# Kernel tuning notes

Hardware: AMD Instinct MI355X
Metric: run time of the kernel (lower is better)

## Reference

```python
import jax, jax.numpy as jnp
import numpy as np

M, B, T, C, H, HS = 2, 8, 1024, 512, 8, 64
EPS = 1e-5

NAMES = ['x','sa_kw1','sa_kb1','sa_kw2','sa_qw1','sa_qb1','sa_qw2','sa_vw1','sa_vb1','sa_vw2',
         'sa_pw1','sa_pb1','sa_pw2','sa_pb2','ff_w1','ff_b1','ff_w2','ff_b2',
         'ln1_g','ln1_b','ln2_g','ln2_b','lnc_g','lnc_b',
         'ca_qw','ca_kvw','ca_pw1','ca_pb1','ca_pw2','ca_pb2']


def setup_inputs() -> dict:
    key = jax.random.key(0)
    it = iter(jax.random.split(key, 40))
    def w(shape, s=0.02):
        return jax.random.normal(next(it), shape, jnp.float32) * s
    d = {}
    d['x'] = jax.random.normal(next(it), (M, B, T, C), jnp.float32)
    # self-attention heads: Linear(C,HS//2)+bias -> tanh -> Linear(HS//2,HS) no bias, stacked over (M,H)
    for nm in ('k', 'q', 'v'):
        d['sa_%sw1' % nm] = w((M, H, C, HS // 2))
        d['sa_%sb1' % nm] = jnp.zeros((M, H, HS // 2), jnp.float32)
        d['sa_%sw2' % nm] = w((M, H, HS // 2, HS))
    # MHA output proj: Linear(H*HS,C//2)->tanh->Linear(C//2,C)
    d['sa_pw1'] = w((M, H * HS, C // 2)); d['sa_pb1'] = jnp.zeros((M, C // 2), jnp.float32)
    d['sa_pw2'] = w((M, C // 2, C));      d['sa_pb2'] = jnp.zeros((M, C), jnp.float32)
    # feed-forward
    d['ff_w1'] = w((M, C, 4 * C)); d['ff_b1'] = jnp.zeros((M, 4 * C), jnp.float32)
    d['ff_w2'] = w((M, 4 * C, C)); d['ff_b2'] = jnp.zeros((M, C), jnp.float32)
    # layernorms
    for nm in ('ln1', 'ln2', 'lnc'):
        d[nm + '_g'] = jnp.ones((M, C), jnp.float32)
        d[nm + '_b'] = jnp.zeros((M, C), jnp.float32)
    # cross-attention: per head q proj (no bias), per-kv-modality kv proj (no bias, 2*HS)
    d['ca_qw'] = w((M, H, C, HS))
    d['ca_kvw'] = w((M, H, M - 1, C, 2 * HS))
    d['ca_pw1'] = w((M, H * HS, C // 2)); d['ca_pb1'] = jnp.zeros((M, C // 2), jnp.float32)
    d['ca_pw2'] = w((M, C // 2, C));      d['ca_pb2'] = jnp.zeros((M, C), jnp.float32)
    return d


def _ln(x, g, b):
    mu = x.mean(-1, keepdims=True)
    var = ((x - mu) ** 2).mean(-1, keepdims=True)
    return (x - mu) * jax.lax.rsqrt(var + EPS) * g + b


def _attend(q, k, v, mask):
    # q,k,v: (B,H,T,HS); causal masked softmax attention
    aff = jnp.einsum('bhtd,bhsd->bhts', q, k) * (HS ** -0.5)
    aff = jnp.where(mask, aff, -jnp.inf)
    return jnp.einsum('bhts,bhsd->bhtd', jax.nn.softmax(aff, axis=-1), v)


def _merge(o):
    # (B,H,T,HS) -> (B,T,H*HS), matching torch.cat over heads
    return o.transpose(0, 2, 1, 3).reshape(o.shape[0], o.shape[2], -1)


def _forward(p):
    mask = jnp.tril(jnp.ones((T, T), bool))
    x = p['x']
    attended = []
    for i in range(M):  # fixed small modality loop
        xi = x[i]
        h = _ln(xi, p['ln1_g'][i], p['ln1_b'][i])
        def hm(w1, b1, w2):
            # batched over heads: Linear->tanh->Linear
            z = jnp.tanh(jnp.einsum('btc,hce->bhte', h, w1) + b1[:, None, :])
            return jnp.einsum('bhte,hed->bhtd', z, w2)
        o = _attend(hm(p['sa_qw1'][i], p['sa_qb1'][i], p['sa_qw2'][i]),
                    hm(p['sa_kw1'][i], p['sa_kb1'][i], p['sa_kw2'][i]),
                    hm(p['sa_vw1'][i], p['sa_vb1'][i], p['sa_vw2'][i]), mask)
        o = jnp.tanh(_merge(o) @ p['sa_pw1'][i] + p['sa_pb1'][i]) @ p['sa_pw2'][i] + p['sa_pb2'][i]
        xi = xi + o
        h2 = _ln(xi, p['ln2_g'][i], p['ln2_b'][i])
        xi = xi + (jax.nn.relu(h2 @ p['ff_w1'][i] + p['ff_b1'][i]) @ p['ff_w2'][i] + p['ff_b2'][i])
        attended.append(xi)
    outs = []
    for i in range(M):
        xi = attended[i]
        hq = _ln(xi, p['lnc_g'][i], p['lnc_b'][i])
        q = jnp.einsum('btc,hcd->bhtd', hq, p['ca_qw'][i])
        acc = 0.0
        for jidx, j in enumerate([j for j in range(M) if j != i]):
            kv = jnp.einsum('btc,hcd->bhtd', attended[j], p['ca_kvw'][i][:, jidx])
            k, v = jnp.split(kv, 2, axis=-1)
            acc = acc + _attend(q, k, v, mask)
        o = jnp.tanh(_merge(acc) @ p['ca_pw1'][i] + p['ca_pb1'][i]) @ p['ca_pw2'][i] + p['ca_pb2'][i]
        outs.append(xi + o)
    return jnp.stack(outs)


def reference(x, sa_kw1, sa_kb1, sa_kw2, sa_qw1, sa_qb1, sa_qw2, sa_vw1, sa_vb1, sa_vw2,
              sa_pw1, sa_pb1, sa_pw2, sa_pb2, ff_w1, ff_b1, ff_w2, ff_b2,
              ln1_g, ln1_b, ln2_g, ln2_b, lnc_g, lnc_b,
              ca_qw, ca_kvw, ca_pw1, ca_pb1, ca_pw2, ca_pb2):
    args = (x, sa_kw1, sa_kb1, sa_kw2, sa_qw1, sa_qb1, sa_qw2, sa_vw1, sa_vb1, sa_vw2,
            sa_pw1, sa_pb1, sa_pw2, sa_pb2, ff_w1, ff_b1, ff_w2, ff_b2,
            ln1_g, ln1_b, ln2_g, ln2_b, lnc_g, lnc_b,
            ca_qw, ca_kvw, ca_pw1, ca_pb1, ca_pw2, ca_pb2)
    return _forward(dict(zip(NAMES, args)))
```

## Files before the change

### kernel.cpp

```cpp
#include <hip/hip_runtime.h>
#include <hip/hip_bf16.h>

#define DEVI __device__ __forceinline__

typedef __attribute__((ext_vector_type(8))) short short8v;
typedef __attribute__((ext_vector_type(4))) float float4v;
typedef __attribute__((ext_vector_type(16))) float f32x16;

#if defined(__has_builtin)
#if __has_builtin(__builtin_amdgcn_exp2f)
#define EXP2F(x) __builtin_amdgcn_exp2f(x)
#endif
#endif
#ifndef EXP2F
#define EXP2F(x) exp2f(x)
#endif

constexpr int Mm = 2, Bb = 8, Tt = 1024, Cc = 512, Hh = 8, HSs = 64;
constexpr int ROWS = Bb * Tt;
constexpr size_t BTC = (size_t)Bb * Tt * Cc;
constexpr size_t SLAB = (size_t)ROWS * 512;
constexpr size_t KOFF = (size_t)2 * ROWS * 768;
constexpr size_t VOFF = KOFF + 2 * SLAB;
constexpr float SCQ = 0.18033688011112042f;

DEVI short f2bf(float f) {
    __hip_bfloat16 h = __float2bfloat16(f);
    short s; __builtin_memcpy(&s, &h, 2); return s;
}

DEVI float4v mfma16(short8v a, short8v b, float4v c) {
    return __builtin_amdgcn_mfma_f32_16x16x32_bf16(a, b, c, 0, 0, 0);
}
DEVI f32x16 mfma32(short8v a, short8v b, f32x16 c) {
    return __builtin_amdgcn_mfma_f32_32x32x16_bf16(a, b, c, 0, 0, 0);
}

DEVI void gload_lds16(const short* g, short* l) {
    __builtin_amdgcn_global_load_lds(
        (const __attribute__((address_space(1))) void*)g,
        (__attribute__((address_space(3))) void*)l, 16, 0, 0);
}

__global__ __launch_bounds__(256) void transpose_cvt(const float* __restrict__ src,
                                                     short* __restrict__ dst,
                                                     int K, int N, size_t moff, size_t hoff) {
    __shared__ float t[32][33];
    int k0 = blockIdx.x * 32, n0 = blockIdx.y * 32;
    int z = blockIdx.z;
    size_t so = (size_t)z * K * N;
    short* d = dst + (size_t)(z >> 3) * moff + (size_t)(z & 7) * hoff;
    int tx = threadIdx.x, ty = threadIdx.y;
#pragma unroll
    for (int i = 0; i < 32; i += 8)
        t[ty + i][tx] = src[so + (size_t)(k0 + ty + i) * N + n0 + tx];
    __syncthreads();
#pragma unroll
    for (int i = 0; i < 32; i += 8)
        d[(size_t)(n0 + ty + i) * K + k0 + tx] = f2bf(t[tx][ty + i]);
}

__global__ __launch_bounds__(256) void bias_cat3(const float* __restrict__ q,
                                                 const float* __restrict__ k,
                                                 const float* __restrict__ v,
                                                 float* __restrict__ o) {
    int m = blockIdx.x, t = threadIdx.x;
    o[m * 768 + t]       = q[m * 256 + t];
    o[m * 768 + 256 + t] = k[m * 256 + t];
    o[m * 768 + 512 + t] = v[m * 256 + t];
}

__global__ __launch_bounds__(256) void vtrans(const short* __restrict__ V,
                                              short* __restrict__ VT,
                                              int vrs, int hs, long long vzs) {
    __shared__ short t[32][33];
    int t0 = blockIdx.x * 32, d0 = blockIdx.y * 32;
    int z = blockIdx.z, mod = z >> 6, bh = z & 63, b = bh >> 3, h = bh & 7;
    const short* src = V + (long long)mod * vzs + (size_t)b * Tt * vrs + h * hs;
    short* dst = VT + (size_t)z * 65536;
    int tx = threadIdx.x, ty = threadIdx.y;
#pragma unroll
    for (int i = 0; i < 32; i += 8)
        t[ty + i][tx] = src[(size_t)(t0 + ty + i) * vrs + d0 + tx];
    __syncthreads();
#pragma unroll
    for (int i = 0; i < 32; i += 8)
        dst[(size_t)(d0 + ty + i) * Tt + t0 + tx] = t[tx][ty + i];
}

__global__ __launch_bounds__(256) void ln_kernel(const float* __restrict__ x,
                                                 const float* __restrict__ g,
                                                 const float* __restrict__ b,
                                                 short* __restrict__ out, size_t xzs) {
    __shared__ float ssum[4], ssq[4];
    int z = blockIdx.y;
    x += z * xzs; g += z * Cc; b += z * Cc; out += z * SLAB;
    int row = blockIdx.x, tid = threadIdx.x;
    const float* xr = x + (size_t)row * Cc;
    float v0 = xr[tid], v1 = xr[tid + 256];
    float s = v0 + v1, q = v0 * v0 + v1 * v1;
#pragma unroll
    for (int o = 1; o < 64; o <<= 1) { s += __shfl_xor(s, o, 64); q += __shfl_xor(q, o, 64); }
    int w = tid >> 6;
    if ((tid & 63) == 0) { ssum[w] = s; ssq[w] = q; }
    __syncthreads();
    s = ssum[0] + ssum[1] + ssum[2] + ssum[3];
    q = ssq[0] + ssq[1] + ssq[2] + ssq[3];
    float mu = s * (1.f / Cc);
    float var = q * (1.f / Cc) - mu * mu;
    float rs = rsqrtf(var + 1e-5f);
    short* orow = out + (size_t)row * Cc;
    orow[tid]       = f2bf((v0 - mu) * rs * g[tid]       + b[tid]);
    orow[tid + 256] = f2bf((v1 - mu) * rs * g[tid + 256] + b[tid + 256]);
}

template<int ACT, bool BIAS, bool RES, bool WF, bool WB>
__global__ __launch_bounds__(256, 2) void gemm3(
    const short* __restrict__ A, int lda, long long a_zs,
    const short* __restrict__ Wt, int ldw, long long w_zs,
    const float* __restrict__ bias, long long bias_zs,
    const float* __restrict__ res, long long res_zs,
    float* __restrict__ outF, long long outF_zs,
    short* __restrict__ outB, long long outB_zs,
    int ldc, int K, float oscale) {
    constexpr int BM = 128, BN = 128, BK = 64;
    __shared__ short As[2][BM][BK];
    __shared__ short Bs[2][BN][BK];
    long long z = blockIdx.z;
    A += z * a_zs; Wt += z * w_zs;
    if (BIAS) bias += z * bias_zs;
    if (RES)  res  += z * res_zs;
    if (WF)   outF += z * outF_zs;
    if (WB)   outB += z * outB_zs;
    int m0 = blockIdx.x * BM, n0 = blockIdx.y * BN;
    int tid = threadIdx.x, wv = tid >> 6, l = tid & 63;
    int lq = l & 31, hi = l >> 5;
    int wm = wv & 1, wn = wv >> 1;
    f32x16 acc[2][2] = {};
    int lrow = l >> 3;
    int gcol = (l & 7) ^ lrow;

    auto STAGE = [&](int bi, int k0) {
#pragma unroll
        for (int c = 0; c < 4; c++) {
            int ch = wv + c * 4;
            gload_lds16(&A[(size_t)(m0 + ch * 8 + lrow) * lda + k0 + gcol * 8],
                        &As[bi][ch * 8][0]);
        }
#pragma unroll
        for (int c = 0; c < 4; c++) {
            int ch = wv + c * 4;
            gload_lds16(&Wt[(size_t)(n0 + ch * 8 + lrow) * ldw + k0 + gcol * 8],
                        &Bs[bi][ch * 8][0]);
        }
    };

    STAGE(0, 0);
    __syncthreads();
    int NT = K / BK;
    for (int t = 0; t < NT; t++) {
        int cur = t & 1;
        if (t + 1 < NT) STAGE(cur ^ 1, (t + 1) * BK);
        const short (*Ac)[BK] = As[cur];
        const short (*Bc)[BK] = Bs[cur];
#pragma unroll
        for (int ks = 0; ks < 4; ks++) {
            int g = (ks * 2 + hi) ^ (lq & 7);
            short8v af[2], bf[2];
#pragma unroll
            for (int i = 0; i < 2; i++)
                af[i] = *(const short8v*)&Ac[wm * 64 + i * 32 + lq][g * 8];
#pragma unroll
            for (int j = 0; j < 2; j++)
                bf[j] = *(const short8v*)&Bc[wn * 64 + j * 32 + lq][g * 8];
#pragma unroll
            for (int i = 0; i < 2; i++)
#pragma unroll
                for (int j = 0; j < 2; j++)
                    acc[i][j] = mfma32(af[i], bf[j], acc[i][j]);
        }
        __syncthreads();
    }
#pragma unroll
    for (int i = 0; i < 2; i++) {
#pragma unroll
        for (int j = 0; j < 2; j++) {
            int col = n0 + wn * 64 + j * 32 + lq;
            float bv = BIAS ? bias[col] : 0.f;
#pragma unroll
            for (int r = 0; r < 16; r++) {
                int row = m0 + wm * 64 + i * 32 + 4 * hi + (r & 3) + 8 * (r >> 2);
                float v = acc[i][j][r] * oscale + bv;
                if (ACT == 1) v = tanhf(v);
                if (ACT == 2) v = fmaxf(v, 0.f);
                size_t idx = (size_t)row * ldc + col;
                if (RES) v += res[idx];
                if (WF) outF[idx] = v;
                if (WB) outB[idx] = f2bf(v);
            }
        }
    }
}

template<int BM, int BN, int ACT, bool BIAS, bool RES, bool WF, bool WB>
__global__ __launch_bounds__(256, 2) void gemm2(
    const short* __restrict__ A, int lda, long long a_zs,
    const short* __restrict__ Wt, int ldw, long long w_zs,
    const float* __restrict__ bias, long long bias_zs,
    const float* __restrict__ res, long long res_zs,
    float* __restrict__ outF, long long outF_zs,
    short* __restrict__ outB, long long outB_zs,
    int ldc, int K, float oscale) {
    constexpr int BK = 64;
    __shared__ short As[BM][BK];
    __shared__ short Bs[BN][BK];
    long long z = blockIdx.z;
    A += z * a_zs; Wt += z * w_zs;
    if (BIAS) bias += z * bias_zs;
    if (RES)  res  += z * res_zs;
    if (WF)   outF += z * outF_zs;
    if (WB)   outB += z * outB_zs;
    int m0 = blockIdx.x * BM, n0 = blockIdx.y * BN;
    int tid = threadIdx.x, wv = tid >> 6, l = tid & 63, lr = l & 15, lg = l >> 4;
    constexpr int WM = BM / 2, WN = BN / 2;
    int wm = wv & 1, wn = wv >> 1;
    constexpr int AI = WM / 16, BJ = WN / 16;
    float4v acc[AI][BJ] = {};
    int lrow = l >> 3;
    int gcol = (l & 7) ^ lrow;
    constexpr int CHA = BM / 8, CHB = BN / 8;
    for (int k0 = 0; k0 < K; k0 += BK) {
        __syncthreads();
#pragma unroll
        for (int c = 0; c < CHA / 4; c++) {
            int ch = wv + c * 4;
            gload_lds16(&A[(size_t)(m0 + ch * 8 + lrow) * lda + k0 + gcol * 8],
                        &As[ch * 8][0]);
        }
#pragma unroll
        for (int c = 0; c < CHB / 4; c++) {
            int ch = wv + c * 4;
            gload_lds16(&Wt[(size_t)(n0 + ch * 8 + lrow) * ldw + k0 + gcol * 8],
                        &Bs[ch * 8][0]);
        }
        __syncthreads();
#pragma unroll
        for (int kk = 0; kk < 2; kk++) {
            int g = (kk * 4 + lg) ^ (lr & 7);
            short8v af[AI], bfv[BJ];
#pragma unroll
            for (int i = 0; i < AI; i++)
                af[i] = *(const short8v*)&As[wm * WM + i * 16 + lr][g * 8];
#pragma unroll
            for (int j = 0; j < BJ; j++)
                bfv[j] = *(const short8v*)&Bs[wn * WN + j * 16 + lr][g * 8];
#pragma unroll
            for (int i = 0; i < AI; i++)
#pragma unroll
                for (int j = 0; j < BJ; j++)
                    acc[i][j] = mfma16(af[i], bfv[j], acc[i][j]);
        }
    }
#pragma unroll
    for (int i = 0; i < AI; i++) {
#pragma unroll
        for (int j = 0; j < BJ; j++) {
            int col = n0 + wn * WN + j * 16 + lr;
            float bv = BIAS ? bias[col] : 0.f;
#pragma unroll
            for (int r = 0; r < 4; r++) {
                int row = m0 + wm * WM + i * 16 + lg * 4 + r;
                float v = acc[i][j][r] * oscale + bv;
                if (ACT == 1) v = tanhf(v);
                if (ACT == 2) v = fmaxf(v, 0.f);
                size_t idx = (size_t)row * ldc + col;
                if (RES) v += res[idx];
                if (WF) outF[idx] = v;
                if (WB) outB[idx] = f2bf(v);
            }
        }
    }
}

__global__ __launch_bounds__(256) void proj2(const short* __restrict__ Z,
                                             const short* __restrict__ W2,
                                             short* __restrict__ Qo,
                                             short* __restrict__ Ko,
                                             short* __restrict__ VTo,
                                             float qscale) {
    __shared__ short As[64][40], Ws[64][40];
    __shared__ short Tv[64][72];
    int zz = blockIdx.y, t = zz >> 4, m = (zz >> 3) & 1, h = zz & 7;
    int m0 = blockIdx.x * 64;
    const short* Ap = Z + (size_t)m * ((size_t)ROWS * 768) + t * 256 + h * 32;
    const short* Wp = W2 + (size_t)zz * 2048;
    float sc = (t == 0) ? qscale : 1.0f;
    int tid = threadIdx.x, w = tid >> 6, l = tid & 63, lr = l & 15, lg = l >> 4;
    int r = tid >> 2, c = (tid & 3) * 8;
    *(short8v*)&As[r][c] = *(const short8v*)&Ap[(size_t)(m0 + r) * 768 + c];
    *(short8v*)&Ws[r][c] = *(const short8v*)&Wp[r * 32 + c];
    __syncthreads();
    short8v af = *(const short8v*)&As[w * 16 + lr][lg * 8];
    float4v acc[4] = {};
#pragma unroll
    for (int j = 0; j < 4; j++) {
        short8v bf = *(const short8v*)&Ws[j * 16 + lr][lg * 8];
        acc[j] = mfma16(af, bf, acc[j]);
    }
    if (t < 2) {
        short* Op = (t == 0 ? Qo : Ko) + (size_t)m * SLAB + h * 64;
#pragma unroll
        for (int j = 0; j < 4; j++)
#pragma unroll
            for (int rr = 0; rr < 4; rr++)
                Op[(size_t)(m0 + w * 16 + lg * 4 + rr) * 512 + j * 16 + lr] =
                    f2bf(acc[j][rr] * sc);
    } else {
#pragma unroll
        for (int j = 0; j < 4; j++)
#pragma unroll
            for (int rr = 0; rr < 4; rr++)
                Tv[j * 16 + lr][w * 16 + lg * 4 + rr] = f2bf(acc[j][rr]);
        __syncthreads();
        int b = m0 >> 10, trow0 = m0 & 1023;
        int z64 = m * 64 + b * 8 + h;
        short* dst = VTo + (size_t)z64 * 65536;
        int d = w * 16 + (l >> 2), toff = (l & 3) * 16;
        *(short8v*)&dst[(size_t)d * Tt + trow0 + toff]     = *(const short8v*)&Tv[d][toff];
        *(short8v*)&dst[(size_t)d * Tt + trow0 + toff + 8] = *(const short8v*)&Tv[d][toff + 8];
    }
}

__global__ __launch_bounds__(512, 4) void flash_attn4(
    const short* __restrict__ Q, const short* __restrict__ K,
    const short* __restrict__ VT, short* __restrict__ O,
    int krs, int khs, long long qzs, long long kzs, long long vtzs, long long ozs)
{
    __shared__ short Ks[2][64][64];
    __shared__ short Vs[2][64][64];
    int id = blockIdx.x;
    int bh = id & 63, mod = (id >> 6) & 1, p = (id >> 7) & 3;
    Q += (long long)mod * qzs; K += (long long)mod * kzs;
    VT += (long long)mod * vtzs; O += (long long)mod * ozs;
    int b = bh >> 3, h = bh & 7;
    int tid = threadIdx.x, w = tid >> 6, l = tid & 63;
    int lq = l & 31, hi = l >> 5;
    int strip = (w < 4) ? p : 7 - p;
    int qwb = strip * 128 + (w & 3) * 32;
    int qabs = qwb + lq;
    const short* Qp = Q + (size_t)b * Tt * Cc + h * HSs;
    const short* Kp = K + (size_t)b * Tt * krs + h * khs;
    const short* Vp = VT + (size_t)bh * HSs * Tt;
    short* Op = O + (size_t)b * Tt * Cc + h * HSs;

    short8v qf[4];
#pragma unroll
    for (int c = 0; c < 4; c++)
        qf[c] = *(const short8v*)&Qp[(size_t)qabs * Cc + (c * 2 + hi) * 8];

    f32x16 oacc[2] = {};
    float mrun = -1e30f, lrun = 0.f;
    int nk = 2 * (7 - p) + 2;
    short8v pk, pv;

    auto LOADT = [&](int kb) {
        int r = tid >> 3, cg = (tid & 7) ^ (r & 7);
        pk = *(const short8v*)&Kp[(size_t)(kb + r) * krs + cg * 8];
        pv = *(const short8v*)&Vp[(size_t)r * Tt + kb + cg * 8];
    };
    auto STORET = [&](int bi) {
        int r = tid >> 3, cp = tid & 7;
        *(short8v*)&Ks[bi][r][cp * 8] = pk;
        *(short8v*)&Vs[bi][r][cp * 8] = pv;
    };

    LOADT(0); STORET(0); __syncthreads();

    for (int t = 0; t < nk; t++) {
        int cur = t & 1, kb = t * 64;
        bool pre = (t + 1 < nk);
        if (pre) LOADT(kb + 64);
        if (kb <= qwb + 31) {
            bool full = (kb + 63 <= qwb);
            f32x16 st[2] = {};
            __builtin_amdgcn_s_setprio(1);
#pragma unroll
            for (int kh = 0; kh < 2; kh++) {
#pragma unroll
                for (int cc = 0; cc < 4; cc++) {
                    int r = kh * 32 + lq;
                    int cp = (cc * 2 + hi) ^ (r & 7);
                    short8v af = *(const short8v*)&Ks[cur][r][cp * 8];
                    st[kh] = mfma32(af, qf[cc], st[kh]);
                }
            }
            __builtin_amdgcn_s_setprio(0);
            float pr[32];
            if (full) {
#pragma unroll
                for (int kh = 0; kh < 2; kh++)
#pragma unroll
                    for (int r = 0; r < 16; r++) pr[kh * 16 + r] = st[kh][r];
            } else {
#pragma unroll
                for (int kh = 0; kh < 2; kh++)
#pragma unroll
                    for (int r = 0; r < 16; r++) {
                        int kabs = kb + kh * 32 + (r & 3) + 8 * (r >> 2) + 4 * hi;
                        pr[kh * 16 + r] = (kabs <= qabs) ? st[kh][r] : -3.0e38f;
                    }
            }
            float t16[16];
#pragma unroll
            for (int i = 0; i < 16; i++) t16[i] = fmaxf(pr[i], pr[i + 16]);
#pragma unroll
            for (int i = 0; i < 8; i++) t16[i] = fmaxf(t16[i], t16[i + 8]);
            float mx = fmaxf(fmaxf(fmaxf(t16[0], t16[4]), fmaxf(t16[1], t16[5])),
                             fmaxf(fmaxf(t16[2], t16[6]), fmaxf(t16[3], t16[7])));
            mx = fmaxf(mx, __shfl_xor(mx, 32));
            if (!__all(mx <= mrun + 11.5f)) {
                float mn = fmaxf(mrun, mx);
                float al = EXP2F(mrun - mn);
                mrun = mn;
                lrun *= al;
#pragma unroll
                for (int dh = 0; dh < 2; dh++)
#pragma unroll
                    for (int r = 0; r < 16; r++) oacc[dh][r] *= al;
            }
#pragma unroll
            for (int i = 0; i < 32; i++) pr[i] = EXP2F(pr[i] - mrun);
            float s16[16];
#pragma unroll
            for (int i = 0; i < 16; i++) s16[i] = pr[i] + pr[i + 16];
#pragma unroll
            for (int i = 0; i < 8; i++) s16[i] = s16[i] + s16[i + 8];
            float rsum = ((s16[0] + s16[4]) + (s16[1] + s16[5])) +
                         ((s16[2] + s16[6]) + (s16[3] + s16[7]));
            rsum += __shfl_xor(rsum, 32);
            lrun += rsum;
#pragma unroll
            for (int ks = 0; ks < 4; ks++) {
                unsigned x0, x1, y0, y1;
                asm("v_cvt_pk_bf16_f32 %0, %1, %2" : "=v"(x0) : "v"(pr[ks*8+0]), "v"(pr[ks*8+1]));
                asm("v_cvt_pk_bf16_f32 %0, %1, %2" : "=v"(x1) : "v"(pr[ks*8+2]), "v"(pr[ks*8+3]));
                asm("v_cvt_pk_bf16_f32 %0, %1, %2" : "=v"(y0) : "v"(pr[ks*8+4]), "v"(pr[ks*8+5]));
                asm("v_cvt_pk_bf16_f32 %0, %1, %2" : "=v"(y1) : "v"(pr[ks*8+6]), "v"(pr[ks*8+7]));
                asm volatile("v_permlane32_swap_b32 %0, %1" : "+v"(x0), "+v"(y0));
                asm volatile("v_permlane32_swap_b32 %0, %1" : "+v"(x1), "+v"(y1));
                union { unsigned u[4]; short8v s; } uu;
                uu.u[0] = x0; uu.u[1] = x1; uu.u[2] = y0; uu.u[3] = y1;
                __builtin_amdgcn_s_setprio(1);
#pragma unroll
                for (int dh = 0; dh < 2; dh++) {
                    int r = dh * 32 + lq;
                    int cp = (ks * 2 + hi) ^ (r & 7);
                    short8v vf = *(const short8v*)&Vs[cur][r][cp * 8];
                    oacc[dh] = mfma32(vf, uu.s, oacc[dh]);
                }
                __builtin_amdgcn_s_setprio(0);
            }
        }
        if (pre) STORET(cur ^ 1);
        __syncthreads();
    }
    float inv = 1.f / lrun;
#pragma unroll
    for (int dh = 0; dh < 2; dh++)
#pragma unroll
        for (int r = 0; r < 16; r += 2) {
            unsigned wds;
            float a0 = oacc[dh][r] * inv, a1 = oacc[dh][r + 1] * inv;
            asm("v_cvt_pk_bf16_f32 %0, %1, %2" : "=v"(wds) : "v"(a0), "v"(a1));
            int d = (r & 3) + 8 * (r >> 2) + 4 * hi + dh * 32;
            *(unsigned*)&Op[(size_t)qabs * Cc + d] = wds;
        }
}

extern "C" void kernel_launch(void* const* d_in, const int* in_sizes, int n_in,
                              void* d_out, int out_size, void* d_ws, size_t ws_size,
                              hipStream_t stream) {
    (void)in_sizes; (void)n_in; (void)out_size; (void)ws_size;
    const float* X     = (const float*)d_in[0];
    const float* saKW1 = (const float*)d_in[1];
    const float* saKB1 = (const float*)d_in[2];
    const float* saKW2 = (const float*)d_in[3];
    const float* saQW1 = (const float*)d_in[4];
    const float* saQB1 = (const float*)d_in[5];
    const float* saQW2 = (const float*)d_in[6];
    const float* saVW1 = (const float*)d_in[7];
    const float* saVB1 = (const float*)d_in[8];
    const float* saVW2 = (const float*)d_in[9];
    const float* saPW1 = (const float*)d_in[10];
    const float* saPB1 = (const float*)d_in[11];
    const float* saPW2 = (const float*)d_in[12];
    const float* saPB2 = (const float*)d_in[13];
    const float* ffW1  = (const float*)d_in[14];
    const float* ffB1  = (const float*)d_in[15];
    const float* ffW2  = (const float*)d_in[16];
    const float* ffB2  = (const float*)d_in[17];
    const float* ln1g  = (const float*)d_in[18];
    const float* ln1b  = (const float*)d_in[19];
    const float* ln2g  = (const float*)d_in[20];
    const float* ln2b  = (const float*)d_in[21];
    const float* lncg  = (const float*)d_in[22];
    const float* lncb  = (const float*)d_in[23];
    const float* caQW  = (const float*)d_in[24];
    const float* caKVW = (const float*)d_in[25];
    const float* caPW1 = (const float*)d_in[26];
    const float* caPB1 = (const float*)d_in[27];
    const float* caPW2 = (const float*)d_in[28];
    const float* caPB2 = (const float*)d_in[29];
    float* OUT = (float*)d_out;

    char* ws = (char*)d_ws;
    size_t cur = 0;
    auto alloc = [&](size_t bytes) -> char* {
        char* p = ws + cur; cur += (bytes + 255) & ~(size_t)255; return p;
    };

    short* WT = (short*)alloc((size_t)7700480 * 2);
    size_t wo = 0;
    auto wslot = [&](size_t e) -> short* { short* p = WT + wo; wo += e; return p; };
    short* w_qkv1 = wslot(786432);
    short* w_qkv2 = wslot(98304);
    short* w_pw1 = wslot(262144); short* w_pw2 = wslot(262144);
    short* w_ff1 = wslot(2097152); short* w_ff2 = wslot(2097152);
    short* w_caq = wslot(524288);  short* w_cakv = wslot(1048576);
    short* w_cp1 = wslot(262144);  short* w_cp2 = wslot(262144);
    float* bqkv = (float*)alloc(2 * 768 * 4);

    short* Hb  = (short*)alloc(2 * SLAB * 2);
    short* Qb  = (short*)alloc(2 * SLAB * 2);
    short* Obf = (short*)alloc(2 * SLAB * 2);
    short* Fb  = (short*)alloc((size_t)2 * ROWS * 2048 * 2);
    short* AB  = (short*)alloc(2 * SLAB * 2);
    short* VTb = Hb;
    short* P1b = Hb;
    short* Kb = Fb + KOFF;

    dim3 tb32(32, 8, 1);
    auto TC = [&](const float* s, short* d, int K, int N, int slices, size_t moff, size_t hoff) {
        transpose_cvt<<<dim3(K / 32, N / 32, slices), tb32, 0, stream>>>(s, d, K, N, moff, hoff);
    };
    TC(saQW1, w_qkv1,          512, 32, 16, 393216, 16384);
    TC(saKW1, w_qkv1 + 131072, 512, 32, 16, 393216, 16384);
    TC(saVW1, w_qkv1 + 262144, 512, 32, 16, 393216, 16384);
    TC(saQW2, w_qkv2,          32, 64, 16, 16384, 2048);
    TC(saKW2, w_qkv2 + 32768,  32, 64, 16, 16384, 2048);
    TC(saVW2, w_qkv2 + 65536,  32, 64, 16, 16384, 2048);
    TC(saPW1, w_pw1, 512, 256, 2, 0, 131072);
    TC(saPW2, w_pw2, 256, 512, 2, 0, 131072);
    TC(ffW1,  w_ff1, 512, 2048, 2, 0, 1048576);
    TC(ffW2,  w_ff2, 2048, 512, 2, 0, 1048576);
    TC(caQW,  w_caq, 512, 64, 16, 262144, 32768);
    TC(caKVW, w_cakv, 512, 128, 16, 524288, 65536);
    TC(caPW1, w_cp1, 512, 256, 2, 0, 131072);
    TC(caPW2, w_cp2, 256, 512, 2, 0, 131072);
    bias_cat3<<<2, 256, 0, stream>>>(saQB1, saKB1, saVB1, bqkv);

    ln_kernel<<<dim3(ROWS, 2), 256, 0, stream>>>(X, ln1g, ln1b, Hb, BTC);
    gemm3<1, true, false, false, true><<<dim3(64, 6, 2), 256, 0, stream>>>(
        Hb, 512, SLAB, w_qkv1, 512, 393216, bqkv, 768,
        nullptr, 0, nullptr, 0, Fb, (long long)ROWS * 768, 768, 512, 1.0f);
    proj2<<<dim3(128, 48), 256, 0, stream>>>(Fb, w_qkv2, Qb, Kb, VTb, SCQ);
    flash_attn4<<<dim3(512), 512, 0, stream>>>(
        Qb, Kb, VTb, Obf, 512, 64, SLAB, SLAB, 4194304, SLAB);
    gemm2<64, 128, 1, true, false, false, true><<<dim3(128, 2, 2), 256, 0, stream>>>(
        Obf, 512, SLAB, w_pw1, 512, 131072, saPB1, 256,
        nullptr, 0, nullptr, 0, P1b, (long long)ROWS * 256, 256, 512, 1.0f);
    gemm3<0, true, true, true, false><<<dim3(64, 4, 2), 256, 0, stream>>>(
        P1b, 256, (long long)ROWS * 256, w_pw2, 256, 131072, saPB2, 512,
        X, BTC, OUT, BTC, nullptr, 0, 512, 256, 1.0f);
    ln_kernel<<<dim3(ROWS, 2), 256, 0, stream>>>(OUT, ln2g, ln2b, Hb, BTC);
    gemm3<2, true, false, false, true><<<dim3(64, 16, 2), 256, 0, stream>>>(
        Hb, 512, SLAB, w_ff1, 512, 1048576, ffB1, 2048,
        nullptr, 0, nullptr, 0, Fb, (long long)ROWS * 2048, 2048, 512, 1.0f);
    gemm3<0, true, true, true, true><<<dim3(64, 4, 2), 256, 0, stream>>>(
        Fb, 2048, (long long)ROWS * 2048, w_ff2, 2048, 1048576, ffB2, 512,
        OUT, BTC, OUT, BTC, AB, SLAB, 512, 2048, 1.0f);

    ln_kernel<<<dim3(ROWS, 2), 256, 0, stream>>>(OUT, lncg, lncb, Hb, BTC);
    gemm3<0, false, false, false, true><<<dim3(64, 4, 2), 256, 0, stream>>>(
        Hb, 512, SLAB, w_caq, 512, 262144, nullptr, 0,
        nullptr, 0, nullptr, 0, Qb, SLAB, 512, 512, SCQ);
    gemm3<0, false, false, false, true><<<dim3(64, 8, 2), 256, 0, stream>>>(
        AB + SLAB, 512, -(long long)SLAB, w_cakv, 512, 524288, nullptr, 0,
        nullptr, 0, nullptr, 0, Fb, (long long)ROWS * 1024, 1024, 512, 1.0f);
    vtrans<<<dim3(32, 2, 128), tb32, 0, stream>>>(Fb + 64, VTb, 1024, 128, (long long)ROWS * 1024);
    flash_attn4<<<dim3(512), 512, 0, stream>>>(
        Qb, Fb, VTb, Obf, 1024, 128, SLAB, (long long)ROWS * 1024, 4194304, SLAB);
    gemm2<64, 128, 1, true, false, false, true><<<dim3(128, 2, 2), 256, 0, stream>>>(
        Obf, 512, SLAB, w_cp1, 512, 131072, caPB1, 256,
        nullptr, 0, nullptr, 0, P1b, (long long)ROWS * 256, 256, 512, 1.0f);
    gemm3<0, true, true, true, false><<<dim3(64, 4, 2), 256, 0, stream>>>(
        P1b, 256, (long long)ROWS * 256, w_cp2, 256, 131072, caPB2, 512,
        OUT, BTC, OUT, BTC, nullptr, 0, 512, 256, 1.0f);
}
```

Measured before the change: 407.5 us.

## Batch weight transposes into one launch, vectorize layernorm, retile GEMMs with gemm2

```diff
diff --git a/kernel.cpp b/kernel.cpp
--- a/kernel.cpp
+++ b/kernel.cpp
@@ -4,6 +4,7 @@
 #define DEVI __device__ __forceinline__
 
 typedef __attribute__((ext_vector_type(8))) short short8v;
+typedef __attribute__((ext_vector_type(4))) short short4v;
 typedef __attribute__((ext_vector_type(4))) float float4v;
 typedef __attribute__((ext_vector_type(16))) float f32x16;
 
@@ -42,22 +43,36 @@
         (__attribute__((address_space(3))) void*)l, 16, 0, 0);
 }
 
-__global__ __launch_bounds__(256) void transpose_cvt(const float* __restrict__ src,
-                                                     short* __restrict__ dst,
-                                                     int K, int N, size_t moff, size_t hoff) {
+struct TDesc {
+    const float* src; short* dst;
+    int K, N;
+    long long moff, hoff;
+    int base;
+};
+struct TPack { TDesc d[14]; };
+
+__global__ __launch_bounds__(256) void transpose_all(TPack p) {
     __shared__ float t[32][33];
-    int k0 = blockIdx.x * 32, n0 = blockIdx.y * 32;
-    int z = blockIdx.z;
-    size_t so = (size_t)z * K * N;
-    short* d = dst + (size_t)(z >> 3) * moff + (size_t)(z & 7) * hoff;
-    int tx = threadIdx.x, ty = threadIdx.y;
+    int bid = blockIdx.x;
+    int di = 0;
+#pragma unroll
+    for (int i = 1; i < 14; i++) if (bid >= p.d[i].base) di = i;
+    TDesc d = p.d[di];
+    int local = bid - d.base;
+    int kb = d.K >> 5, nb = d.N >> 5;
+    int bx = local % kb; int rest = local / kb;
+    int by = rest % nb;  int z = rest / nb;
+    int k0 = bx * 32, n0 = by * 32;
+    size_t so = (size_t)z * d.K * d.N;
+    short* dst = d.dst + (size_t)(z >> 3) * d.moff + (size_t)(z & 7) * d.hoff;
+    int tx = threadIdx.x & 31, ty = threadIdx.x >> 5;
 #pragma unroll
     for (int i = 0; i < 32; i += 8)
-        t[ty + i][tx] = src[so + (size_t)(k0 + ty + i) * N + n0 + tx];
+        t[ty + i][tx] = d.src[so + (size_t)(k0 + ty + i) * d.N + n0 + tx];
     __syncthreads();
 #pragma unroll
     for (int i = 0; i < 32; i += 8)
-        d[(size_t)(n0 + ty + i) * K + k0 + tx] = f2bf(t[tx][ty + i]);
+        dst[(size_t)(n0 + ty + i) * d.K + k0 + tx] = f2bf(t[tx][ty + i]);
 }
 
 __global__ __launch_bounds__(256) void bias_cat3(const float* __restrict__ q,
@@ -92,114 +107,35 @@
                                                  const float* __restrict__ g,
                                                  const float* __restrict__ b,
                                                  short* __restrict__ out, size_t xzs) {
-    __shared__ float ssum[4], ssq[4];
     int z = blockIdx.y;
     x += z * xzs; g += z * Cc; b += z * Cc; out += z * SLAB;
-    int row = blockIdx.x, tid = threadIdx.x;
+    int row = blockIdx.x * 4 + (threadIdx.x >> 6);
+    int l = threadIdx.x & 63;
     const float* xr = x + (size_t)row * Cc;
-    float v0 = xr[tid], v1 = xr[tid + 256];
-    float s = v0 + v1, q = v0 * v0 + v1 * v1;
+    float4 a = *(const float4*)&xr[l * 4];
+    float4 c = *(const float4*)&xr[256 + l * 4];
+    float s = (a.x + a.y) + (a.z + a.w) + (c.x + c.y) + (c.z + c.w);
+    float q = (a.x * a.x + a.y * a.y) + (a.z * a.z + a.w * a.w) +
+              (c.x * c.x + c.y * c.y) + (c.z * c.z + c.w * c.w);
 #pragma unroll
     for (int o = 1; o < 64; o <<= 1) { s += __shfl_xor(s, o, 64); q += __shfl_xor(q, o, 64); }
-    int w = tid >> 6;
-    if ((tid & 63) == 0) { ssum[w] = s; ssq[w] = q; }
-    __syncthreads();
-    s = ssum[0] + ssum[1] + ssum[2] + ssum[3];
-    q = ssq[0] + ssq[1] + ssq[2] + ssq[3];
     float mu = s * (1.f / Cc);
     float var = q * (1.f / Cc) - mu * mu;
     float rs = rsqrtf(var + 1e-5f);
+    float4 ga = *(const float4*)&g[l * 4],   gc = *(const float4*)&g[256 + l * 4];
+    float4 ba = *(const float4*)&b[l * 4],   bc = *(const float4*)&b[256 + l * 4];
+    short4v o1, o2;
+    o1[0] = f2bf((a.x - mu) * rs * ga.x + ba.x);
+    o1[1] = f2bf((a.y - mu) * rs * ga.y + ba.y);
+    o1[2] = f2bf((a.z - mu) * rs * ga.z + ba.z);
+    o1[3] = f2bf((a.w - mu) * rs * ga.w + ba.w);
+    o2[0] = f2bf((c.x - mu) * rs * gc.x + bc.x);
+    o2[1] = f2bf((c.y - mu) * rs * gc.y + bc.y);
+    o2[2] = f2bf((c.z - mu) * rs * gc.z + bc.z);
+    o2[3] = f2bf((c.w - mu) * rs * gc.w + bc.w);
     short* orow = out + (size_t)row * Cc;
-    orow[tid]       = f2bf((v0 - mu) * rs * g[tid]       + b[tid]);
-    orow[tid + 256] = f2bf((v1 - mu) * rs * g[tid + 256] + b[tid + 256]);
-}
-
-template<int ACT, bool BIAS, bool RES, bool WF, bool WB>
-__global__ __launch_bounds__(256, 2) void gemm3(
-    const short* __restrict__ A, int lda, long long a_zs,
-    const short* __restrict__ Wt, int ldw, long long w_zs,
-    const float* __restrict__ bias, long long bias_zs,
-    const float* __restrict__ res, long long res_zs,
-    float* __restrict__ outF, long long outF_zs,
-    short* __restrict__ outB, long long outB_zs,
-    int ldc, int K, float oscale) {
-    constexpr int BM = 128, BN = 128, BK = 64;
-    __shared__ short As[2][BM][BK];
-    __shared__ short Bs[2][BN][BK];
-    long long z = blockIdx.z;
-    A += z * a_zs; Wt += z * w_zs;
-    if (BIAS) bias += z * bias_zs;
-    if (RES)  res  += z * res_zs;
-    if (WF)   outF += z * outF_zs;
-    if (WB)   outB += z * outB_zs;
-    int m0 = blockIdx.x * BM, n0 = blockIdx.y * BN;
-    int tid = threadIdx.x, wv = tid >> 6, l = tid & 63;
-    int lq = l & 31, hi = l >> 5;
-    int wm = wv & 1, wn = wv >> 1;
-    f32x16 acc[2][2] = {};
-    int lrow = l >> 3;
-    int gcol = (l & 7) ^ lrow;
-
-    auto STAGE = [&](int bi, int k0) {
-#pragma unroll
-        for (int c = 0; c < 4; c++) {
-            int ch = wv + c * 4;
-            gload_lds16(&A[(size_t)(m0 + ch * 8 + lrow) * lda + k0 + gcol * 8],
-                        &As[bi][ch * 8][0]);
-        }
-#pragma unroll
-        for (int c = 0; c < 4; c++) {
-            int ch = wv + c * 4;
-            gload_lds16(&Wt[(size_t)(n0 + ch * 8 + lrow) * ldw + k0 + gcol * 8],
-                        &Bs[bi][ch * 8][0]);
-        }
-    };
-
-    STAGE(0, 0);
-    __syncthreads();
-    int NT = K / BK;
-    for (int t = 0; t < NT; t++) {
-        int cur = t & 1;
-        if (t + 1 < NT) STAGE(cur ^ 1, (t + 1) * BK);
-        const short (*Ac)[BK] = As[cur];
-        const short (*Bc)[BK] = Bs[cur];
-#pragma unroll
-        for (int ks = 0; ks < 4; ks++) {
-            int g = (ks * 2 + hi) ^ (lq & 7);
-            short8v af[2], bf[2];
-#pragma unroll
-            for (int i = 0; i < 2; i++)
-                af[i] = *(const short8v*)&Ac[wm * 64 + i * 32 + lq][g * 8];
-#pragma unroll
-            for (int j = 0; j < 2; j++)
-                bf[j] = *(const short8v*)&Bc[wn * 64 + j * 32 + lq][g * 8];
-#pragma unroll
-            for (int i = 0; i < 2; i++)
-#pragma unroll
-                for (int j = 0; j < 2; j++)
-                    acc[i][j] = mfma32(af[i], bf[j], acc[i][j]);
-        }
-        __syncthreads();
-    }
-#pragma unroll
-    for (int i = 0; i < 2; i++) {
-#pragma unroll
-        for (int j = 0; j < 2; j++) {
-            int col = n0 + wn * 64 + j * 32 + lq;
-            float bv = BIAS ? bias[col] : 0.f;
-#pragma unroll
-            for (int r = 0; r < 16; r++) {
-                int row = m0 + wm * 64 + i * 32 + 4 * hi + (r & 3) + 8 * (r >> 2);
-                float v = acc[i][j][r] * oscale + bv;
-                if (ACT == 1) v = tanhf(v);
-                if (ACT == 2) v = fmaxf(v, 0.f);
-                size_t idx = (size_t)row * ldc + col;
-                if (RES) v += res[idx];
-                if (WF) outF[idx] = v;
-                if (WB) outB[idx] = f2bf(v);
-            }
-        }
-    }
+    *(short4v*)&orow[l * 4]       = o1;
+    *(short4v*)&orow[256 + l * 4] = o2;
 }
 
 template<int BM, int BN, int ACT, bool BIAS, bool RES, bool WF, bool WB>
@@ -270,6 +206,94 @@
 #pragma unroll
             for (int r = 0; r < 4; r++) {
                 int row = m0 + wm * WM + i * 16 + lg * 4 + r;
+                float v = acc[i][j][r] * oscale + bv;
+                if (ACT == 1) v = tanhf(v);
+                if (ACT == 2) v = fmaxf(v, 0.f);
+                size_t idx = (size_t)row * ldc + col;
+                if (RES) v += res[idx];
+                if (WF) outF[idx] = v;
+                if (WB) outB[idx] = f2bf(v);
+            }
+        }
+    }
+}
+
+template<int ACT, bool BIAS, bool RES, bool WF, bool WB>
+__global__ __launch_bounds__(256, 2) void gemm3(
+    const short* __restrict__ A, int lda, long long a_zs,
+    const short* __restrict__ Wt, int ldw, long long w_zs,
+    const float* __restrict__ bias, long long bias_zs,
+    const float* __restrict__ res, long long res_zs,
+    float* __restrict__ outF, long long outF_zs,
+    short* __restrict__ outB, long long outB_zs,
+    int ldc, int K, float oscale) {
+    constexpr int BM = 128, BN = 128, BK = 64;
+    __shared__ short As[2][BM][BK];
+    __shared__ short Bs[2][BN][BK];
+    long long z = blockIdx.z;
+    A += z * a_zs; Wt += z * w_zs;
+    if (BIAS) bias += z * bias_zs;
+    if (RES)  res  += z * res_zs;
+    if (WF)   outF += z * outF_zs;
+    if (WB)   outB += z * outB_zs;
+    int m0 = blockIdx.x * BM, n0 = blockIdx.y * BN;
+    int tid = threadIdx.x, wv = tid >> 6, l = tid & 63;
+    int lq = l & 31, hi = l >> 5;
+    int wm = wv & 1, wn = wv >> 1;
+    f32x16 acc[2][2] = {};
+    int lrow = l >> 3;
+    int gcol = (l & 7) ^ lrow;
+
+    auto STAGE = [&](int bi, int k0) {
+#pragma unroll
+        for (int c = 0; c < 4; c++) {
+            int ch = wv + c * 4;
+            gload_lds16(&A[(size_t)(m0 + ch * 8 + lrow) * lda + k0 + gcol * 8],
+                        &As[bi][ch * 8][0]);
+        }
+#pragma unroll
+        for (int c = 0; c < 4; c++) {
+            int ch = wv + c * 4;
+            gload_lds16(&Wt[(size_t)(n0 + ch * 8 + lrow) * ldw + k0 + gcol * 8],
+                        &Bs[bi][ch * 8][0]);
+        }
+    };
+
+    STAGE(0, 0);
+    __syncthreads();
+    int NT = K / BK;
+    for (int t = 0; t < NT; t++) {
+        int cur = t & 1;
+        if (t + 1 < NT) STAGE(cur ^ 1, (t + 1) * BK);
+        const short (*Ac)[BK] = As[cur];
+        const short (*Bc)[BK] = Bs[cur];
+#pragma unroll
+        for (int ks = 0; ks < 4; ks++) {
+            int g = (ks * 2 + hi) ^ (lq & 7);
+            short8v af[2], bf[2];
+#pragma unroll
+            for (int i = 0; i < 2; i++)
+                af[i] = *(const short8v*)&Ac[wm * 64 + i * 32 + lq][g * 8];
+#pragma unroll
+            for (int j = 0; j < 2; j++)
+                bf[j] = *(const short8v*)&Bc[wn * 64 + j * 32 + lq][g * 8];
+#pragma unroll
+            for (int i = 0; i < 2; i++)
+#pragma unroll
+                for (int j = 0; j < 2; j++)
+                    acc[i][j] = mfma32(af[i], bf[j], acc[i][j]);
+        }
+        __syncthreads();
+    }
+#pragma unroll
+    for (int i = 0; i < 2; i++) {
+#pragma unroll
+        for (int j = 0; j < 2; j++) {
+            int col = n0 + wn * 64 + j * 32 + lq;
+            float bv = BIAS ? bias[col] : 0.f;
+#pragma unroll
+            for (int r = 0; r < 16; r++) {
+                int row = m0 + wm * 64 + i * 32 + 4 * hi + (r & 3) + 8 * (r >> 2);
                 float v = acc[i][j][r] * oscale + bv;
                 if (ACT == 1) v = tanhf(v);
                 if (ACT == 2) v = fmaxf(v, 0.f);
@@ -539,28 +563,34 @@
     short* P1b = Hb;
     short* Kb = Fb + KOFF;
 
+    TPack tp;
+    int base = 0, ti = 0;
+    auto addT = [&](const float* s, short* d, int K, int N, int slices,
+                    long long moff, long long hoff) {
+        tp.d[ti++] = TDesc{s, d, K, N, moff, hoff, base};
+        base += (K / 32) * (N / 32) * slices;
+    };
+    addT(saQW1, w_qkv1,          512, 32, 16, 393216, 16384);
+    addT(saKW1, w_qkv1 + 131072, 512, 32, 16, 393216, 16384);
+    addT(saVW1, w_qkv1 + 262144, 512, 32, 16, 393216, 16384);
+    addT(saQW2, w_qkv2,          32, 64, 16, 16384, 2048);
+    addT(saKW2, w_qkv2 + 32768,  32, 64, 16, 16384, 2048);
+    addT(saVW2, w_qkv2 + 65536,  32, 64, 16, 16384, 2048);
+    addT(saPW1, w_pw1, 512, 256, 2, 0, 131072);
+    addT(saPW2, w_pw2, 256, 512, 2, 0, 131072);
+    addT(ffW1,  w_ff1, 512, 2048, 2, 0, 1048576);
+    addT(ffW2,  w_ff2, 2048, 512, 2, 0, 1048576);
+    addT(caQW,  w_caq, 512, 64, 16, 262144, 32768);
+    addT(caKVW, w_cakv, 512, 128, 16, 524288, 65536);
+    addT(caPW1, w_cp1, 512, 256, 2, 0, 131072);
+    addT(caPW2, w_cp2, 256, 512, 2, 0, 131072);
+    transpose_all<<<dim3(base), 256, 0, stream>>>(tp);
+    bias_cat3<<<2, 256, 0, stream>>>(saQB1, saKB1, saVB1, bqkv);
+
     dim3 tb32(32, 8, 1);
-    auto TC = [&](const float* s, short* d, int K, int N, int slices, size_t moff, size_t hoff) {
-        transpose_cvt<<<dim3(K / 32, N / 32, slices), tb32, 0, stream>>>(s, d, K, N, moff, hoff);
-    };
-    TC(saQW1, w_qkv1,          512, 32, 16, 393216, 16384);
-    TC(saKW1, w_qkv1 + 131072, 512, 32, 16, 393216, 16384);
-    TC(saVW1, w_qkv1 + 262144, 512, 32, 16, 393216, 16384);
-    TC(saQW2, w_qkv2,          32, 64, 16, 16384, 2048);
-    TC(saKW2, w_qkv2 + 32768,  32, 64, 16, 16384, 2048);
-    TC(saVW2, w_qkv2 + 65536,  32, 64, 16, 16384, 2048);
-    TC(saPW1, w_pw1, 512, 256, 2, 0, 131072);
-    TC(saPW2, w_pw2, 256, 512, 2, 0, 131072);
-    TC(ffW1,  w_ff1, 512, 2048, 2, 0, 1048576);
-    TC(ffW2,  w_ff2, 2048, 512, 2, 0, 1048576);
-    TC(caQW,  w_caq, 512, 64, 16, 262144, 32768);
-    TC(caKVW, w_cakv, 512, 128, 16, 524288, 65536);
-    TC(caPW1, w_cp1, 512, 256, 2, 0, 131072);
-    TC(caPW2, w_cp2, 256, 512, 2, 0, 131072);
-    bias_cat3<<<2, 256, 0, stream>>>(saQB1, saKB1, saVB1, bqkv);
-
-    ln_kernel<<<dim3(ROWS, 2), 256, 0, stream>>>(X, ln1g, ln1b, Hb, BTC);
-    gemm3<1, true, false, false, true><<<dim3(64, 6, 2), 256, 0, stream>>>(
+
+    ln_kernel<<<dim3(ROWS / 4, 2), 256, 0, stream>>>(X, ln1g, ln1b, Hb, BTC);
+    gemm2<128, 128, 1, true, false, false, true><<<dim3(64, 6, 2), 256, 0, stream>>>(
         Hb, 512, SLAB, w_qkv1, 512, 393216, bqkv, 768,
         nullptr, 0, nullptr, 0, Fb, (long long)ROWS * 768, 768, 512, 1.0f);
     proj2<<<dim3(128, 48), 256, 0, stream>>>(Fb, w_qkv2, Qb, Kb, VTb, SCQ);
@@ -569,22 +599,22 @@
     gemm2<64, 128, 1, true, false, false, true><<<dim3(128, 2, 2), 256, 0, stream>>>(
         Obf, 512, SLAB, w_pw1, 512, 131072, saPB1, 256,
         nullptr, 0, nullptr, 0, P1b, (long long)ROWS * 256, 256, 512, 1.0f);
-    gemm3<0, true, true, true, false><<<dim3(64, 4, 2), 256, 0, stream>>>(
+    gemm2<64, 128, 0, true, true, true, false><<<dim3(128, 4, 2), 256, 0, stream>>>(
         P1b, 256, (long long)ROWS * 256, w_pw2, 256, 131072, saPB2, 512,
         X, BTC, OUT, BTC, nullptr, 0, 512, 256, 1.0f);
-    ln_kernel<<<dim3(ROWS, 2), 256, 0, stream>>>(OUT, ln2g, ln2b, Hb, BTC);
-    gemm3<2, true, false, false, true><<<dim3(64, 16, 2), 256, 0, stream>>>(
+    ln_kernel<<<dim3(ROWS / 4, 2), 256, 0, stream>>>(OUT, ln2g, ln2b, Hb, BTC);
+    gemm2<128, 128, 2, true, false, false, true><<<dim3(64, 16, 2), 256, 0, stream>>>(
         Hb, 512, SLAB, w_ff1, 512, 1048576, ffB1, 2048,
         nullptr, 0, nullptr, 0, Fb, (long long)ROWS * 2048, 2048, 512, 1.0f);
     gemm3<0, true, true, true, true><<<dim3(64, 4, 2), 256, 0, stream>>>(
         Fb, 2048, (long long)ROWS * 2048, w_ff2, 2048, 1048576, ffB2, 512,
         OUT, BTC, OUT, BTC, AB, SLAB, 512, 2048, 1.0f);
 
-    ln_kernel<<<dim3(ROWS, 2), 256, 0, stream>>>(OUT, lncg, lncb, Hb, BTC);
-    gemm3<0, false, false, false, true><<<dim3(64, 4, 2), 256, 0, stream>>>(
+    ln_kernel<<<dim3(ROWS / 4, 2), 256, 0, stream>>>(OUT, lncg, lncb, Hb, BTC);
+    gemm2<64, 128, 0, false, false, false, true><<<dim3(128, 4, 2), 256, 0, stream>>>(
         Hb, 512, SLAB, w_caq, 512, 262144, nullptr, 0,
         nullptr, 0, nullptr, 0, Qb, SLAB, 512, 512, SCQ);
-    gemm3<0, false, false, false, true><<<dim3(64, 8, 2), 256, 0, stream>>>(
+    gemm2<128, 128, 0, false, false, false, true><<<dim3(64, 8, 2), 256, 0, stream>>>(
         AB + SLAB, 512, -(long long)SLAB, w_cakv, 512, 524288, nullptr, 0,
         nullptr, 0, nullptr, 0, Fb, (long long)ROWS * 1024, 1024, 512, 1.0f);
     vtrans<<<dim3(32, 2, 128), tb32, 0, stream>>>(Fb + 64, VTb, 1024, 128, (long long)ROWS * 1024);
@@ -593,7 +623,7 @@
     gemm2<64, 128, 1, true, false, false, true><<<dim3(128, 2, 2), 256, 0, stream>>>(
         Obf, 512, SLAB, w_cp1, 512, 131072, caPB1, 256,
         nullptr, 0, nullptr, 0, P1b, (long long)ROWS * 256, 256, 512, 1.0f);
-    gemm3<0, true, true, true, false><<<dim3(64, 4, 2), 256, 0, stream>>>(
+    gemm2<64, 128, 0, true, true, true, false><<<dim3(128, 4, 2), 256, 0, stream>>>(
         P1b, 256, (long long)ROWS * 256, w_cp2, 256, 131072, caPB2, 512,
         OUT, BTC, OUT, BTC, nullptr, 0, 512, 256, 1.0f);
 }
```

Result: faster. 355.3 us (-12.8%).
